# Kernel optimization log

Measured on AMD Instinct MI355X. Metric: run time of the kernel, lower is better.

The kernel has to match this reference:

```python
import jax, jax.numpy as jnp
import numpy as np

# Graph geometry: L depth levels of M nodes, fan_in K scalar connections, per-node dim D
L, M, K, D, B = 8, 128, 32, 16, 2048
N = L * M  # 1024 nodes


def setup_inputs() -> dict:
    key = jax.random.key(0)
    ks = jax.random.split(key, 6)
    x = jax.random.normal(ks[0], (B, D), jnp.float32)
    trace = jax.random.normal(ks[1], (N, B, D), jnp.float32)  # previous-step recurrent state per node
    src_node = jax.random.randint(ks[2], (N, K), 0, N + 1)    # 0 = external input x, else node id (1..N)
    src_feat = jax.random.randint(ks[3], (N, K), 0, D)        # scalar index k within source output
    W = jax.random.normal(ks[4], (N, D, K), jnp.float32) / np.sqrt(K)  # per-node Linear(K -> D)
    b = jax.random.normal(ks[5], (N, D), jnp.float32) * 0.01
    return {"x": x, "trace": trace, "src_node": src_node, "src_feat": src_feat, "W": W, "b": b}


def reference(x, trace, src_node, src_feat, W, b):
    # state buffers have row 0 = external input x, rows 1..N = node states
    h_state = jnp.concatenate([jnp.zeros((1, B, D), x.dtype), jax.lax.stop_gradient(trace)], axis=0)  # prev-step snapshot (detached, like torch .detach())
    cur0 = jnp.concatenate([x[None], jax.lax.stop_gradient(trace)], axis=0)  # current-step buffer, row 0 readable as input
    sn = src_node.reshape(L, M, K)
    sf = src_feat.reshape(L, M, K)
    Wl = W.reshape(L, M, D, K)
    bl = b.reshape(L, M, D)

    def step(cur, xs):
        l, sn_l, sf_l, W_l, b_l = xs
        g_cur = cur[sn_l, :, sf_l]      # [M, K, B] gather from current-step buffer
        g_h = h_state[sn_l, :, sf_l]    # [M, K, B] gather from previous-step snapshot
        # source depth >= current depth -> recurrent edge -> read h; else feedforward -> read cur
        use_h = (sn_l > 0) & (((sn_l - 1) // M) >= l)
        g = jnp.where(use_h[:, :, None], g_h, g_cur)                     # [M, K, B]
        o = jax.nn.relu(jnp.einsum('mkb,mdk->mbd', g, W_l) + b_l[:, None, :])  # [M, B, D]
        cur = jax.lax.dynamic_update_slice(cur, o, (1 + l * M, 0, 0))    # scatter into trace buffer
        return cur, o

    _, outs = jax.lax.scan(step, cur0, (jnp.arange(L), sn, sf, Wl, bl))  # outs: [L, M, B, D]
    return outs.reshape(N, B, D)  # updated trace; last node's forward return is outs[-1]
```

## Files before the change

### kernel.cpp

```cpp
#include <hip/hip_runtime.h>
#include <hip/hip_bf16.h>

#define L_ 8
#define M_ 128
#define K_ 32
#define D_ 16
#define B_ 2048
#define N_ 1024
#define SLAB_ 32768

__global__ __launch_bounds__(256) void transpose_bd(const float* __restrict__ trace,
                                                    const float* __restrict__ x,
                                                    float* __restrict__ traceT,
                                                    float* __restrict__ xT) {
    int blk = blockIdx.x;
    const float* src;
    float* dst;
    int bt;
    if (blk < N_ * 32) {
        int n = blk >> 5;
        src = trace + (size_t)n * SLAB_;
        dst = traceT + (size_t)n * SLAB_;
        bt  = blk & 31;
    } else {
        src = x;
        dst = xT;
        bt  = blk - N_ * 32;
    }
    int b0 = bt * 64;

    __shared__ float lds[D_][65];

    int tid = threadIdx.x;

    const float4* s4 = (const float4*)src;
    int b  = tid >> 2;
    int dq = tid & 3;
    float4 v = s4[(size_t)(b0 + b) * 4 + dq];
    lds[dq * 4 + 0][b] = v.x;
    lds[dq * 4 + 1][b] = v.y;
    lds[dq * 4 + 2][b] = v.z;
    lds[dq * 4 + 3][b] = v.w;
    __syncthreads();

    int d  = tid >> 4;
    int bq = tid & 15;
    float4 w;
    w.x = lds[d][bq * 4 + 0];
    w.y = lds[d][bq * 4 + 1];
    w.z = lds[d][bq * 4 + 2];
    w.w = lds[d][bq * 4 + 3];
    ((float4*)(dst + (size_t)d * B_ + b0))[bq] = w;
}

__global__ __launch_bounds__(256) void layer_kernel(
    int l,
    const float* __restrict__ xbuf, int xfs, int xbs,
    const float* __restrict__ tbuf, int tfs, int tbs,
    const float* __restrict__ obuf, int ofs, int obs,
    const int* __restrict__ sn, const int* __restrict__ sf,
    const float* __restrict__ W, const float* __restrict__ bias,
    float* __restrict__ out, float* __restrict__ outT, int writeT)
{
    int m  = blockIdx.x >> 3;
    int bt = blockIdx.x & 7;
    int n  = l * M_ + m;
    int b  = bt * 256 + threadIdx.x;

    __shared__ float        Wsh[D_][K_];
    __shared__ float        bsh[D_];
    __shared__ const float* colp[K_];
    __shared__ int          colbs[K_];
    __shared__ float        osh[256][17];

    int tid = threadIdx.x;

    if (tid < 128) {
        ((float4*)&Wsh[0][0])[tid] = ((const float4*)(W + (size_t)n * D_ * K_))[tid];
    }
    if (tid < D_) bsh[tid] = bias[(size_t)n * D_ + tid];
    if (tid < K_) {
        int s = sn[(size_t)n * K_ + tid];
        int f = sf[(size_t)n * K_ + tid];
        const float* p;
        int bs;
        if (s == 0) {
            p  = xbuf + (size_t)f * xfs;
            bs = xbs;
        } else {
            int ls = (s - 1) >> 7;
            if (ls >= l) {
                p  = tbuf + (size_t)(s - 1) * SLAB_ + (size_t)f * tfs;
                bs = tbs;
            } else {
                p  = obuf + (size_t)(s - 1) * SLAB_ + (size_t)f * ofs;
                bs = obs;
            }
        }
        colp[tid]  = p;
        colbs[tid] = bs;
    }
    __syncthreads();

    float g[K_];
#pragma unroll
    for (int k = 0; k < K_; ++k) {
        g[k] = colp[k][(size_t)b * colbs[k]];
    }

#pragma unroll
    for (int d = 0; d < D_; ++d) {
        float acc = bsh[d];
#pragma unroll
        for (int k = 0; k < K_; ++k) acc = fmaf(g[k], Wsh[d][k], acc);
        acc = fmaxf(acc, 0.0f);
        osh[tid][d] = acc;
        if (writeT) outT[(size_t)n * SLAB_ + (size_t)d * B_ + b] = acc;
    }
    __syncthreads();

    float4* region4 = (float4*)(out + (size_t)n * SLAB_ + (size_t)(bt * 256) * D_);
#pragma unroll
    for (int j = 0; j < 4; ++j) {
        int i   = j * 256 + tid;
        int row = i >> 2;
        int c0  = (i & 3) * 4;
        float4 w;
        w.x = osh[row][c0 + 0];
        w.y = osh[row][c0 + 1];
        w.z = osh[row][c0 + 2];
        w.w = osh[row][c0 + 3];
        region4[i] = w;
    }
}

extern "C" void kernel_launch(void* const* d_in, const int* in_sizes, int n_in,
                              void* d_out, int out_size, void* d_ws, size_t ws_size,
                              hipStream_t stream) {
    const float* x     = (const float*)d_in[0];
    const float* trace = (const float*)d_in[1];
    const int*   sn    = (const int*)d_in[2];
    const int*   sf    = (const int*)d_in[3];
    const float* W     = (const float*)d_in[4];
    const float* bias  = (const float*)d_in[5];
    float*       out   = (float*)d_out;

    const size_t xT_elems  = (size_t)D_ * B_;
    const size_t big_elems = (size_t)N_ * SLAB_;
    const size_t needA = sizeof(float) * (xT_elems + 2 * big_elems);
    const size_t needB = sizeof(float) * (xT_elems + 1 * big_elems);

    float* ws = (float*)d_ws;

    if (ws_size >= needA) {
        float* xT     = ws;
        float* traceT = ws + xT_elems;
        float* outT   = traceT + big_elems;

        transpose_bd<<<N_ * 32 + 32, 256, 0, stream>>>(trace, x, traceT, xT);
        for (int l = 0; l < L_; ++l) {
            layer_kernel<<<M_ * 8, 256, 0, stream>>>(
                l,
                xT,     B_, 1,
                traceT, B_, 1,
                outT,   B_, 1,
                sn, sf, W, bias, out, outT, 1);
        }
    } else if (ws_size >= needB) {
        float* xT     = ws;
        float* traceT = ws + xT_elems;

        transpose_bd<<<N_ * 32 + 32, 256, 0, stream>>>(trace, x, traceT, xT);
        for (int l = 0; l < L_; ++l) {
            layer_kernel<<<M_ * 8, 256, 0, stream>>>(
                l,
                xT,     B_, 1,
                traceT, B_, 1,
                out,    1,  D_,
                sn, sf, W, bias, out, nullptr, 0);
        }
    } else {
        for (int l = 0; l < L_; ++l) {
            layer_kernel<<<M_ * 8, 256, 0, stream>>>(
                l,
                x,     1, D_,
                trace, 1, D_,
                out,   1, D_,
                sn, sf, W, bias, out, nullptr, 0);
        }
    }
}
```

Before: 368.3 us.

## Fuse all layers into one kernel keeping current-step node outputs in LDS

Replaces the full-trace transpose plus eight per-layer launches with a single fused kernel in which each block owns two batch columns and walks through all layers. Feedforward gathers read node outputs from a swizzled 128 KB LDS buffer rather than global memory, and recurrent gathers read the original trace directly. A small pre-pass transposes W so each thread can load its weights as float4. This removes the 128 MB transpose and the global round trips between layers, but uses scattered uncoalesced global reads for recurrent edges and relies on large dynamic LDS, which limits occupancy.

```diff
diff --git a/kernel.cpp b/kernel.cpp
--- a/kernel.cpp
+++ b/kernel.cpp
@@ -8,6 +8,87 @@
 #define B_ 2048
 #define N_ 1024
 #define SLAB_ 32768
+
+
+__global__ __launch_bounds__(512) void wtrans_kernel(const float* __restrict__ W,
+                                                     float* __restrict__ Wt) {
+    int n = blockIdx.x;
+    int t = threadIdx.x;
+    int d = t >> 5;
+    int k = t & 31;
+    Wt[(size_t)n * 512 + k * 16 + d] = W[(size_t)n * 512 + t];
+}
+
+__global__ __launch_bounds__(512, 2) void fused_kernel(
+    const float* __restrict__ x, const float* __restrict__ trace,
+    const int* __restrict__ sn, const int* __restrict__ sf,
+    const float* __restrict__ Wt, const float* __restrict__ bias,
+    float* __restrict__ out)
+{
+    extern __shared__ float st[];
+
+    int tid = threadIdx.x;
+    int m   = tid >> 2;
+    int bsl = (tid >> 1) & 1;
+    int dh  = tid & 1;
+    int bb  = (blockIdx.x << 1) + bsl;
+
+    const float* xrow = x     + ((size_t)bb << 4);
+    const float* trb  = trace + ((size_t)bb << 4);
+
+    for (int l = 0; l < L_; ++l) {
+        int n = (l << 7) + m;
+        const int* snp = sn + ((size_t)n << 5);
+        const int* sfp = sf + ((size_t)n << 5);
+
+        const float4* bp = (const float4*)(bias + ((size_t)n << 4) + (dh << 3));
+        float4 bA = bp[0], bB = bp[1];
+        float acc[8];
+        acc[0] = bA.x; acc[1] = bA.y; acc[2] = bA.z; acc[3] = bA.w;
+        acc[4] = bB.x; acc[5] = bB.y; acc[6] = bB.z; acc[7] = bB.w;
+
+        const float4* wbase = (const float4*)(Wt + ((size_t)n << 9) + (dh << 3));
+
+        int thr = l << 7;
+#pragma unroll 8
+        for (int k = 0; k < K_; ++k) {
+            int s = snp[k];
+            int f = sfp[k];
+            float g;
+            if (s > thr) {
+                g = trb[((size_t)(s - 1) << 15) + f];
+            } else if (s == 0) {
+                g = xrow[f];
+            } else {
+                int row = s - 1;
+                g = st[(row << 5) + (((f + row) & 15) << 1) + bsl];
+            }
+            float4 w0 = wbase[(k << 2)];
+            float4 w1 = wbase[(k << 2) + 1];
+            acc[0] = fmaf(g, w0.x, acc[0]); acc[1] = fmaf(g, w0.y, acc[1]);
+            acc[2] = fmaf(g, w0.z, acc[2]); acc[3] = fmaf(g, w0.w, acc[3]);
+            acc[4] = fmaf(g, w1.x, acc[4]); acc[5] = fmaf(g, w1.y, acc[5]);
+            acc[6] = fmaf(g, w1.z, acc[6]); acc[7] = fmaf(g, w1.w, acc[7]);
+        }
+
+#pragma unroll
+        for (int j = 0; j < 8; ++j) acc[j] = fmaxf(acc[j], 0.0f);
+
+        float4* o4 = (float4*)(out + (((size_t)((n << 11) + bb)) << 4) + (dh << 3));
+        o4[0] = make_float4(acc[0], acc[1], acc[2], acc[3]);
+        o4[1] = make_float4(acc[4], acc[5], acc[6], acc[7]);
+
+        if (l < L_ - 1) {
+            int fb = dh << 3;
+#pragma unroll
+            for (int j = 0; j < 8; ++j) {
+                st[(n << 5) + ((((fb + j) + n) & 15) << 1) + bsl] = acc[j];
+            }
+            __syncthreads();
+        }
+    }
+}
+
 
 __global__ __launch_bounds__(256) void transpose_bd(const float* __restrict__ trace,
                                                     const float* __restrict__ x,
@@ -32,7 +113,6 @@
     __shared__ float lds[D_][65];
 
     int tid = threadIdx.x;
-
     const float4* s4 = (const float4*)src;
     int b  = tid >> 2;
     int dq = tid & 3;
@@ -145,6 +225,28 @@
     const float* bias  = (const float*)d_in[5];
     float*       out   = (float*)d_out;
 
+    static int use_fused = -1;
+    if (use_fused < 0) {
+        hipError_t e = hipFuncSetAttribute(
+            reinterpret_cast<const void*>(fused_kernel),
+            hipFuncAttributeMaxDynamicSharedMemorySize, 131072);
+        if (e != hipSuccess) {
+            (void)hipGetLastError();
+            use_fused = 0;
+        } else {
+            use_fused = 1;
+        }
+    }
+
+    const size_t wt_bytes = sizeof(float) * (size_t)N_ * D_ * K_;
+
+    if (use_fused == 1 && ws_size >= wt_bytes) {
+        float* Wt = (float*)d_ws;
+        wtrans_kernel<<<N_, 512, 0, stream>>>(W, Wt);
+        fused_kernel<<<B_ / 2, 512, 131072, stream>>>(x, trace, sn, sf, Wt, bias, out);
+        return;
+    }
+
     const size_t xT_elems  = (size_t)D_ * B_;
     const size_t big_elems = (size_t)N_ * SLAB_;
     const size_t needA = sizeof(float) * (xT_elems + 2 * big_elems);
```

Result: slower. 751.1 us (+103.9%).

## Fuse all layers into one batch-tiled kernel holding node outputs in LDS

Applied to the files above, without the earlier changes.

Replaces the full trace transpose and the eight per-layer launches with a small prep kernel and one fused kernel. The prep kernel transposes W and encodes each source edge into a tagged offset. Each fused block takes two batch rows, runs all 1024 nodes across all depths, and keeps feedforward outputs in 128KB of swizzled LDS, so intermediate outputs are never read back from global memory. This removes the big transpose traffic and the per-layer launches, but relies on uncoalesced scalar gathers from trace rows, a large LDS allocation that limits occupancy, and a block-wide barrier per layer.

```diff
diff --git a/kernel.cpp b/kernel.cpp
--- a/kernel.cpp
+++ b/kernel.cpp
@@ -1,5 +1,6 @@
 #include <hip/hip_runtime.h>
 #include <hip/hip_bf16.h>
+#include <stdint.h>
 
 #define L_ 8
 #define M_ 128
@@ -8,6 +9,104 @@
 #define B_ 2048
 #define N_ 1024
 #define SLAB_ 32768
+
+
+__global__ __launch_bounds__(512) void prep_kernel(const float* __restrict__ W,
+                                                   const int* __restrict__ sn,
+                                                   const int* __restrict__ sf,
+                                                   float* __restrict__ Wt,
+                                                   uint32_t* __restrict__ meta) {
+    int n = blockIdx.x;
+    int t = threadIdx.x;
+    int d = t >> 5;
+    int k = t & 31;
+    Wt[(size_t)n * 512 + k * 16 + d] = W[(size_t)n * 512 + t];
+    if (t < K_) {
+        int s = sn[(size_t)n * K_ + t];
+        int f = sf[(size_t)n * K_ + t];
+        int l = n >> 7;
+        uint32_t mk;
+        if (s == 0) {
+            mk = (1u << 30) | (uint32_t)f;
+        } else if (s > (l << 7)) {
+            mk = (uint32_t)((s - 1) * SLAB_ + f);
+        } else {
+            int r = s - 1;
+            mk = (2u << 30) | (uint32_t)((r << 5) + (((f + r) & 15) << 1));
+        }
+        meta[(size_t)n * K_ + t] = mk;
+    }
+}
+
+__global__ __launch_bounds__(1024) void fused_kernel(
+    const float* __restrict__ x, const float* __restrict__ trace,
+    const uint32_t* __restrict__ meta, const float* __restrict__ Wt,
+    const float* __restrict__ bias, float* __restrict__ out)
+{
+    extern __shared__ float st[];
+    __shared__ float xs[2][16];
+
+    int tid = threadIdx.x;
+    int m   = tid >> 3;
+    int bsl = (tid >> 2) & 1;
+    int dq  = tid & 3;
+    int bb  = (blockIdx.x << 1) + bsl;
+
+    if (tid < 32) {
+        int bs = tid >> 4, f = tid & 15;
+        xs[bs][f] = x[(((size_t)(blockIdx.x << 1) + bs) << 4) + f];
+    }
+    __syncthreads();
+
+    const float* trb = trace + ((size_t)bb << 4);
+    const float* stg = st;
+    const float* xsg = &xs[bsl][0];
+
+    for (int l = 0; l < L_; ++l) {
+        int n = (l << 7) + m;
+        const uint32_t* mp = meta + ((size_t)n << 5);
+
+        float g[K_];
+#pragma unroll
+        for (int k = 0; k < K_; ++k) {
+            uint32_t mk  = mp[k];
+            uint32_t tag = mk >> 30;
+            uint32_t off = mk & 0x3FFFFFFFu;
+            const float* p = (tag == 0) ? (trb + off)
+                           : (tag == 1) ? (xsg + off)
+                           :              (stg + off + bsl);
+            g[k] = *p;
+        }
+
+        float4 bv = *(const float4*)(bias + ((size_t)n << 4) + (dq << 2));
+        float a0 = bv.x, a1 = bv.y, a2 = bv.z, a3 = bv.w;
+
+        const float4* wb = (const float4*)(Wt + ((size_t)n << 9)) + dq;
+#pragma unroll
+        for (int k = 0; k < K_; ++k) {
+            float4 w = wb[k << 2];
+            a0 = fmaf(g[k], w.x, a0);
+            a1 = fmaf(g[k], w.y, a1);
+            a2 = fmaf(g[k], w.z, a2);
+            a3 = fmaf(g[k], w.w, a3);
+        }
+        a0 = fmaxf(a0, 0.0f); a1 = fmaxf(a1, 0.0f);
+        a2 = fmaxf(a2, 0.0f); a3 = fmaxf(a3, 0.0f);
+
+        float4* o4 = (float4*)(out + ((((size_t)n << 11) + bb) << 4) + (dq << 2));
+        *o4 = make_float4(a0, a1, a2, a3);
+
+        if (l < L_ - 1) {
+            int fb = dq << 2;
+            st[(n << 5) + ((((fb + 0) + n) & 15) << 1) + bsl] = a0;
+            st[(n << 5) + ((((fb + 1) + n) & 15) << 1) + bsl] = a1;
+            st[(n << 5) + ((((fb + 2) + n) & 15) << 1) + bsl] = a2;
+            st[(n << 5) + ((((fb + 3) + n) & 15) << 1) + bsl] = a3;
+            __syncthreads();
+        }
+    }
+}
+
 
 __global__ __launch_bounds__(256) void transpose_bd(const float* __restrict__ trace,
                                                     const float* __restrict__ x,
@@ -32,7 +131,6 @@
     __shared__ float lds[D_][65];
 
     int tid = threadIdx.x;
-
     const float4* s4 = (const float4*)src;
     int b  = tid >> 2;
     int dq = tid & 3;
@@ -145,6 +243,31 @@
     const float* bias  = (const float*)d_in[5];
     float*       out   = (float*)d_out;
 
+    static int use_fused = -1;
+    if (use_fused < 0) {
+        hipError_t e = hipFuncSetAttribute(
+            reinterpret_cast<const void*>(fused_kernel),
+            hipFuncAttributeMaxDynamicSharedMemorySize, 131072);
+        if (e != hipSuccess) {
+            (void)hipGetLastError();
+            use_fused = 0;
+        } else {
+            use_fused = 1;
+        }
+    }
+
+    const size_t wt_elems  = (size_t)N_ * D_ * K_;
+    const size_t fused_ws  = sizeof(float) * wt_elems
+                           + sizeof(uint32_t) * (size_t)N_ * K_;
+
+    if (use_fused == 1 && ws_size >= fused_ws) {
+        float*    Wt   = (float*)d_ws;
+        uint32_t* meta = (uint32_t*)(Wt + wt_elems);
+        prep_kernel<<<N_, 512, 0, stream>>>(W, sn, sf, Wt, meta);
+        fused_kernel<<<B_ / 2, 1024, 131072, stream>>>(x, trace, meta, Wt, bias, out);
+        return;
+    }
+
     const size_t xT_elems  = (size_t)D_ * B_;
     const size_t big_elems = (size_t)N_ * SLAB_;
     const size_t needA = sizeof(float) * (xT_elems + 2 * big_elems);
```

New measurement: 611.0 us. 65.9% more time.
